# Kernel tuning notes

Measured on AMD Instinct MI355X. Metric: run time of the kernel, lower is better.

Reference implementation:

```python
import jax, jax.numpy as jnp
import numpy as np

HEADS = 16


def _linear(x, w, b):
    # torch nn.Linear: y = x @ W^T + b, W: (out, in)
    return jnp.einsum('bld,od->blo', x, w) + b


def setup_inputs() -> dict:
    key = jax.random.key(0)
    ks = jax.random.split(key, 11)
    B, L, QD, KVD = 8, 2048, 1024, 1024
    s_in = 1.0 / np.sqrt(QD)
    return {
        'query': jax.random.normal(ks[0], (B, L, QD), jnp.float32),
        'key':   jax.random.normal(ks[1], (B, L, KVD), jnp.float32),
        'value': jax.random.normal(ks[2], (B, L, KVD), jnp.float32),
        'wq_w': jax.random.normal(ks[3], (KVD, QD), jnp.float32) * s_in,
        'wq_b': jnp.zeros((KVD,), jnp.float32),
        'wk_w': jax.random.normal(ks[4], (KVD, KVD), jnp.float32) * s_in,
        'wk_b': jnp.zeros((KVD,), jnp.float32),
        'wv_w': jax.random.normal(ks[5], (KVD, KVD), jnp.float32) * s_in,
        'wv_b': jnp.zeros((KVD,), jnp.float32),
        'fo_w': jax.random.normal(ks[6], (QD, KVD), jnp.float32) * s_in,
        'fo_b': jnp.zeros((QD,), jnp.float32),
    }


def reference(query, key, value, wq_w, wq_b, wk_w, wk_b, wv_w, wv_b, fo_w, fo_b):
    B, Lq, _ = query.shape
    Lk = key.shape[1]
    kvd = wq_w.shape[0]
    head_dim = kvd // HEADS
    # reshape WITHOUT transpose, exactly as the torch source: (B, L, heads, head_dim)
    q = _linear(query, wq_w, wq_b).reshape(B, Lq, HEADS, head_dim)
    k = _linear(key,   wk_w, wk_b).reshape(B, Lk, HEADS, head_dim)
    v = _linear(value, wv_w, wv_b).reshape(B, Lk, HEADS, head_dim)
    scale = 1.0 / jnp.sqrt(jnp.float32(head_dim))
    # Faithful to source: seq axis acts as 'h'; heads axis is contracted (i,j).
    scores = jnp.einsum('bhid,bhjd->bhij', q, k) * scale  # (B, L, heads, heads)
    weights = jax.nn.softmax(scores, axis=-1)
    out = jnp.einsum('bhij,bhjd->bhid', weights, v)       # (B, L, heads, head_dim)
    out = out.reshape(B, Lq, kvd)
    return _linear(out, fo_w, fo_b)
```

## Files before the change

### kernel.cpp

```cpp
#include <hip/hip_runtime.h>
#include <hip/hip_bf16.h>


typedef __attribute__((ext_vector_type(8))) __bf16 bf16x8;
typedef __attribute__((ext_vector_type(4))) float f32x4;

#define BM 128
#define BN 128
#define BK 64

__device__ __forceinline__ float bf2f(ushort u) {
  union { unsigned int i; float f; } c; c.i = ((unsigned int)u) << 16; return c.f;
}
__device__ __forceinline__ ushort f2b(float f) {
  union { float f; unsigned int i; } c; c.f = f;
  unsigned int x = c.i;
  return (ushort)((x + 0x7FFFu + ((x >> 16) & 1u)) >> 16);
}

__global__ __launch_bounds__(256)
void cvt_f32_bf16(const float* __restrict__ s, ushort* __restrict__ d, int n8)
{
  int i = blockIdx.x * 256 + threadIdx.x;
  if (i >= n8) return;
  const float4* sp = reinterpret_cast<const float4*>(s) + (size_t)i * 2;
  float4 a = sp[0], b = sp[1];
  ushort u[8] = { f2b(a.x), f2b(a.y), f2b(a.z), f2b(a.w),
                  f2b(b.x), f2b(b.y), f2b(b.z), f2b(b.w) };
  reinterpret_cast<uint4*>(d)[i] = *reinterpret_cast<uint4*>(u);
}

__global__ __launch_bounds__(256)
void cvt_w3(const float* __restrict__ a, const float* __restrict__ b,
            const float* __restrict__ c, ushort* __restrict__ dst, int n8each)
{
  int i = blockIdx.x * 256 + threadIdx.x;
  if (i >= 3 * n8each) return;
  const float* s; int j;
  if (i < n8each)            { s = a; j = i; }
  else if (i < 2 * n8each)   { s = b; j = i - n8each; }
  else                       { s = c; j = i - 2 * n8each; }
  const float4* sp = reinterpret_cast<const float4*>(s) + (size_t)j * 2;
  float4 x = sp[0], y = sp[1];
  ushort u[8] = { f2b(x.x), f2b(x.y), f2b(x.z), f2b(x.w),
                  f2b(y.x), f2b(y.y), f2b(y.z), f2b(y.w) };
  reinterpret_cast<uint4*>(dst)[i] = *reinterpret_cast<uint4*>(u);
}

__global__ __launch_bounds__(256)
void cvt_wo_perm(const float* __restrict__ w, ushort* __restrict__ o)
{
  int t = blockIdx.x * 256 + threadIdx.x;
  int n  = t >> 7;
  int i8 = (t & 127) << 3;
  int blk = i8 >> 8, g = (i8 >> 6) & 3, c = (i8 >> 2) & 15;
  const float* src = w + (size_t)n * 1024 + 4 * g * 64 + blk * 16 + c;
  ushort u[8];
  #pragma unroll
  for (int j = 0; j < 8; ++j)
    u[j] = f2b(src[(j & 3) * 64 + (j >> 2)]);
  *reinterpret_cast<uint4*>(o + (size_t)n * 1024 + i8) = *reinterpret_cast<uint4*>(u);
}

template<int CMODE>
__global__ __launch_bounds__(512, 2)
void gemm8p(const ushort* __restrict__ A, const ushort* __restrict__ Bw,
            const float* __restrict__ bias, void* __restrict__ Cv,
            int M, int N, int K)
{
  extern __shared__ ushort lds[];

  const int tid  = threadIdx.x;
  const int lane = tid & 63;
  const int wid  = tid >> 6;
  const int wm   = wid >> 2;
  const int wn   = wid & 3;

  const int nwg = gridDim.x * gridDim.y;
  int fid = blockIdx.y * gridDim.x + blockIdx.x;
  if ((nwg & 7) == 0) fid = (fid & 7) * (nwg >> 3) + (fid >> 3);
  const int bx = fid % gridDim.x;
  const int by = fid / gridDim.x;
  const int m0 = by * 256, n0 = bx * 256;

  const int NT = K >> 6;

  const int csw = ((lane & 7) ^ (lane >> 3)) << 3;
  auto STAGE = [&](int h, int kt, int b) {
    const ushort* base = (h >= 2) ? Bw : A;
    const int o0 = (h >= 2) ? n0 : m0;
    const int rl = (h & 1) * 128;
    #pragma unroll
    for (int j = 0; j < 2; ++j) {
      int rt = rl + j * 64 + wid * 8;
      const ushort* src = base + (size_t)(o0 + rt + (lane >> 3)) * K + kt * 64 + csw;
      ushort* dst = lds + b * 32768 + (h >= 2 ? 16384 : 0) + rt * 64;
      __builtin_amdgcn_global_load_lds(
          (const __attribute__((address_space(1))) void*)src,
          (__attribute__((address_space(3))) void*)dst, 16, 0, 0);
    }
  };

  auto LDA = [&](int b, int mi, int kk) -> bf16x8 {
    int row  = (mi & 3) * 16 + wm * 64 + (mi >> 2) * 128 + (lane & 15);
    int slot = kk * 4 + (lane >> 4);
    int byte = row * 128 + (((slot ^ (row & 7)) & 7) << 4);
    return *reinterpret_cast<const bf16x8*>((const char*)(lds + b * 32768) + byte);
  };
  auto LDB = [&](int b, int ni, int kk) -> bf16x8 {
    int row  = (ni & 1) * 16 + wn * 32 + (ni >> 1) * 128 + (lane & 15);
    int slot = kk * 4 + (lane >> 4);
    int byte = row * 128 + (((slot ^ (row & 7)) & 7) << 4);
    return *reinterpret_cast<const bf16x8*>((const char*)(lds + b * 32768 + 16384) + byte);
  };

  f32x4 acc[8][4] = {};
  bf16x8 af[4][2], bf[4][2];

  STAGE(0, 0, 0); STAGE(2, 0, 0); STAGE(3, 0, 0); STAGE(1, 0, 0);
  asm volatile("s_waitcnt vmcnt(4)" ::: "memory");
  __builtin_amdgcn_s_barrier();

  for (int t = 0; t < NT; ++t) {
    const int cur = t & 1;
    const int nxt = cur ^ 1;
    const bool pf = (t + 1) < NT;

    #pragma unroll
    for (int i = 0; i < 4; ++i) { af[i][0] = LDA(cur, i, 0); af[i][1] = LDA(cur, i, 1); }
    #pragma unroll
    for (int n = 0; n < 2; ++n) { bf[n][0] = LDB(cur, n, 0); bf[n][1] = LDB(cur, n, 1); }
    if (pf) { STAGE(0, t + 1, nxt); asm volatile("s_waitcnt vmcnt(4)" ::: "memory"); }
    else    {                       asm volatile("s_waitcnt vmcnt(2)" ::: "memory"); }
    __builtin_amdgcn_s_barrier();
    asm volatile("s_waitcnt lgkmcnt(0)" ::: "memory");
    __builtin_amdgcn_sched_barrier(0);
    __builtin_amdgcn_s_setprio(1);
    #pragma unroll
    for (int i = 0; i < 4; ++i)
      #pragma unroll
      for (int n = 0; n < 2; ++n)
        #pragma unroll
        for (int kk = 0; kk < 2; ++kk)
          acc[i][n] = __builtin_amdgcn_mfma_f32_16x16x32_bf16(af[i][kk], bf[n][kk], acc[i][n], 0, 0, 0);
    __builtin_amdgcn_s_setprio(0);
    __builtin_amdgcn_s_barrier();

    #pragma unroll
    for (int n = 0; n < 2; ++n) { bf[2 + n][0] = LDB(cur, 2 + n, 0); bf[2 + n][1] = LDB(cur, 2 + n, 1); }
    if (pf) { STAGE(2, t + 1, nxt); asm volatile("s_waitcnt vmcnt(4)" ::: "memory"); }
    else    {                       asm volatile("s_waitcnt vmcnt(0)" ::: "memory"); }
    __builtin_amdgcn_s_barrier();
    asm volatile("s_waitcnt lgkmcnt(0)" ::: "memory");
    __builtin_amdgcn_sched_barrier(0);
    __builtin_amdgcn_s_setprio(1);
    #pragma unroll
    for (int i = 0; i < 4; ++i)
      #pragma unroll
      for (int n = 0; n < 2; ++n)
        #pragma unroll
        for (int kk = 0; kk < 2; ++kk)
          acc[i][2 + n] = __builtin_amdgcn_mfma_f32_16x16x32_bf16(af[i][kk], bf[2 + n][kk], acc[i][2 + n], 0, 0, 0);
    __builtin_amdgcn_s_setprio(0);
    __builtin_amdgcn_s_barrier();

    #pragma unroll
    for (int i = 0; i < 4; ++i) { af[i][0] = LDA(cur, 4 + i, 0); af[i][1] = LDA(cur, 4 + i, 1); }
    if (pf) STAGE(3, t + 1, nxt);
    __builtin_amdgcn_s_barrier();
    asm volatile("s_waitcnt lgkmcnt(0)" ::: "memory");
    __builtin_amdgcn_sched_barrier(0);
    __builtin_amdgcn_s_setprio(1);
    #pragma unroll
    for (int i = 0; i < 4; ++i)
      #pragma unroll
      for (int n = 0; n < 2; ++n)
        #pragma unroll
        for (int kk = 0; kk < 2; ++kk)
          acc[4 + i][n] = __builtin_amdgcn_mfma_f32_16x16x32_bf16(af[i][kk], bf[n][kk], acc[4 + i][n], 0, 0, 0);
    __builtin_amdgcn_s_setprio(0);
    __builtin_amdgcn_s_barrier();

    if (pf) { STAGE(1, t + 1, nxt); asm volatile("s_waitcnt vmcnt(4)" ::: "memory"); }
    __builtin_amdgcn_s_barrier();
    __builtin_amdgcn_s_setprio(1);
    #pragma unroll
    for (int i = 0; i < 4; ++i)
      #pragma unroll
      for (int n = 0; n < 2; ++n)
        #pragma unroll
        for (int kk = 0; kk < 2; ++kk)
          acc[4 + i][2 + n] = __builtin_amdgcn_mfma_f32_16x16x32_bf16(af[i][kk], bf[2 + n][kk], acc[4 + i][2 + n], 0, 0, 0);
    __builtin_amdgcn_s_setprio(0);
    __builtin_amdgcn_s_barrier();
  }

  #pragma unroll
  for (int ni = 0; ni < 4; ++ni) {
    int col = n0 + (ni & 1) * 16 + wn * 32 + (ni >> 1) * 128 + (lane & 15);
    float bv = bias[col];
    #pragma unroll
    for (int mi = 0; mi < 8; ++mi) {
      int row0 = m0 + (mi & 3) * 16 + wm * 64 + (mi >> 2) * 128 + ((lane >> 4) << 2);
      #pragma unroll
      for (int q = 0; q < 4; ++q) {
        float v = acc[mi][ni][q] + bv;
        if constexpr (CMODE == 0)
          ((float*)Cv)[(size_t)(row0 + q) * N + col] = v;
        else
          ((ushort*)Cv)[(size_t)(row0 + q) * N + col] = f2b(v);
      }
    }
  }
}

__global__ __launch_bounds__(256)
void attn_mfma2(const ushort* __restrict__ Q, const ushort* __restrict__ Kh,
                const ushort* __restrict__ V, ushort* __restrict__ Ot, int P)
{
  const int lane = threadIdx.x & 63;
  const int wid  = threadIdx.x >> 6;
  const int g = lane >> 4, c = lane & 15;
  const int stride = gridDim.x * 4;

  for (int p = blockIdx.x * 4 + wid; p < P; p += stride) {
    const ushort* qb = Q  + (size_t)p * 1024;
    const ushort* kb = Kh + (size_t)p * 1024;
    const ushort* vb = V  + (size_t)p * 1024;

    bf16x8 qf0 = *reinterpret_cast<const bf16x8*>(qb + c * 64 + g * 8);
    bf16x8 qf1 = *reinterpret_cast<const bf16x8*>(qb + c * 64 + 32 + g * 8);
    bf16x8 kf0 = *reinterpret_cast<const bf16x8*>(kb + c * 64 + g * 8);
    bf16x8 kf1 = *reinterpret_cast<const bf16x8*>(kb + c * 64 + 32 + g * 8);

    f32x4 s = {};
    s = __builtin_amdgcn_mfma_f32_16x16x32_bf16(kf0, qf0, s, 0, 0, 0);
    s = __builtin_amdgcn_mfma_f32_16x16x32_bf16(kf1, qf1, s, 0, 0, 0);

    float s0 = s[0] * 0.125f, s1 = s[1] * 0.125f;
    float s2 = s[2] * 0.125f, s3 = s[3] * 0.125f;
    float m = fmaxf(fmaxf(s0, s1), fmaxf(s2, s3));
    m = fmaxf(m, __shfl_xor(m, 16));
    m = fmaxf(m, __shfl_xor(m, 32));
    float e0 = __expf(s0 - m), e1 = __expf(s1 - m);
    float e2 = __expf(s2 - m), e3 = __expf(s3 - m);
    float sum = e0 + e1 + e2 + e3;
    sum += __shfl_xor(sum, 16);
    sum += __shfl_xor(sum, 32);
    float r = 1.0f / sum;

    uint pk0 = (uint)f2b(e0 * r) | ((uint)f2b(e1 * r) << 16);
    uint pk1 = (uint)f2b(e2 * r) | ((uint)f2b(e3 * r) << 16);

    int srcA = (((2 * g) & 3) << 4) | c;
    int srcB = (((2 * g + 1) & 3) << 4) | c;
    uint a0 = (uint)__shfl((int)pk0, srcA);
    uint a1 = (uint)__shfl((int)pk1, srcA);
    uint a2 = (uint)__shfl((int)pk0, srcB);
    uint a3 = (uint)__shfl((int)pk1, srcB);
    if (g >= 2) { a0 = 0; a1 = 0; a2 = 0; a3 = 0; }
    union { uint u[4]; bf16x8 v; } pa;
    pa.u[0] = a0; pa.u[1] = a1; pa.u[2] = a2; pa.u[3] = a3;

    ushort* ob = Ot + (size_t)p * 1024;
    #pragma unroll
    for (int blk = 0; blk < 4; ++blk) {
      union { ushort u[8]; bf16x8 v; } vf;
      #pragma unroll
      for (int e = 0; e < 8; ++e)
        vf.u[e] = vb[(8 * (g & 1) + e) * 64 + blk * 16 + c];
      f32x4 o = {};
      o = __builtin_amdgcn_mfma_f32_16x16x32_bf16(pa.v, vf.v, o, 0, 0, 0);
      uint lo = (uint)f2b(o[0]) | ((uint)f2b(o[1]) << 16);
      uint hi = (uint)f2b(o[2]) | ((uint)f2b(o[3]) << 16);
      uint2 w2; w2.x = lo; w2.y = hi;
      *reinterpret_cast<uint2*>(ob + blk * 256 + g * 64 + c * 4) = w2;
    }
  }
}

template<bool A_IS_BF16, bool OUT_BF16>
__global__ __launch_bounds__(256)
void gemm_bt(const void* __restrict__ Av, const float* __restrict__ B,
             const float* __restrict__ bias, void* __restrict__ Cv,
             int M, int N, int K)
{
  __shared__ ushort As[BM * BK];
  __shared__ ushort Bs[BN * BK];

  const int tid  = threadIdx.x;
  const int lane = tid & 63;
  const int wid  = tid >> 6;
  const int wr   = wid >> 1;
  const int wc   = wid & 1;
  const int m0   = blockIdx.y * BM;
  const int n0   = blockIdx.x * BN;

  f32x4 acc[4][4] = {};

  const int r   = tid >> 1;
  const int seg = (tid & 1) * 32;

  for (int k0 = 0; k0 < K; k0 += BK) {
    {
      ushort tmp[32];
      if constexpr (A_IS_BF16) {
        const ushort* gA = (const ushort*)Av + (size_t)(m0 + r) * K + k0 + seg;
        #pragma unroll
        for (int u = 0; u < 4; ++u)
          *reinterpret_cast<uint4*>(&tmp[u * 8]) =
              *reinterpret_cast<const uint4*>(gA + u * 8);
      } else {
        const float* gA = (const float*)Av + (size_t)(m0 + r) * K + k0 + seg;
        #pragma unroll
        for (int u = 0; u < 8; ++u) {
          float4 f = *reinterpret_cast<const float4*>(gA + u * 4);
          tmp[u * 4 + 0] = f2b(f.x); tmp[u * 4 + 1] = f2b(f.y);
          tmp[u * 4 + 2] = f2b(f.z); tmp[u * 4 + 3] = f2b(f.w);
        }
      }
      #pragma unroll
      for (int s4 = 0; s4 < 4; ++s4) {
        int slot = (seg >> 3) + s4;
        int byte = r * 128 + ((slot ^ (r & 7)) << 4);
        *reinterpret_cast<uint4*>((char*)As + byte) =
            *reinterpret_cast<uint4*>(&tmp[s4 * 8]);
      }
    }
    {
      const float* gB = B + (size_t)(n0 + r) * K + k0 + seg;
      ushort tmp[32];
      #pragma unroll
      for (int u = 0; u < 8; ++u) {
        float4 f = *reinterpret_cast<const float4*>(gB + u * 4);
        tmp[u * 4 + 0] = f2b(f.x); tmp[u * 4 + 1] = f2b(f.y);
        tmp[u * 4 + 2] = f2b(f.z); tmp[u * 4 + 3] = f2b(f.w);
      }
      #pragma unroll
      for (int s4 = 0; s4 < 4; ++s4) {
        int slot = (seg >> 3) + s4;
        int byte = r * 128 + ((slot ^ (r & 7)) << 4);
        *reinterpret_cast<uint4*>((char*)Bs + byte) =
            *reinterpret_cast<uint4*>(&tmp[s4 * 8]);
      }
    }
    __syncthreads();

    #pragma unroll
    for (int kk = 0; kk < 2; ++kk) {
      const int kbase = kk * 32 + ((lane >> 4) << 3);
      const int slot  = kbase >> 3;
      bf16x8 af[4], bfr[4];
      #pragma unroll
      for (int mi = 0; mi < 4; ++mi) {
        int row = wr * 64 + mi * 16 + (lane & 15);
        af[mi] = *reinterpret_cast<const bf16x8*>(
            (const char*)As + row * 128 + ((slot ^ (row & 7)) << 4));
      }
      #pragma unroll
      for (int ni = 0; ni < 4; ++ni) {
        int row = wc * 64 + ni * 16 + (lane & 15);
        bfr[ni] = *reinterpret_cast<const bf16x8*>(
            (const char*)Bs + row * 128 + ((slot ^ (row & 7)) << 4));
      }
      #pragma unroll
      for (int mi = 0; mi < 4; ++mi)
        #pragma unroll
        for (int ni = 0; ni < 4; ++ni)
          acc[mi][ni] = __builtin_amdgcn_mfma_f32_16x16x32_bf16(
              af[mi], bfr[ni], acc[mi][ni], 0, 0, 0);
    }
    __syncthreads();
  }

  #pragma unroll
  for (int ni = 0; ni < 4; ++ni) {
    int col = n0 + wc * 64 + ni * 16 + (lane & 15);
    float bv = bias[col];
    #pragma unroll
    for (int mi = 0; mi < 4; ++mi) {
      int row0 = m0 + wr * 64 + mi * 16 + ((lane >> 4) << 2);
      #pragma unroll
      for (int q = 0; q < 4; ++q) {
        float v = acc[mi][ni][q] + bv;
        if constexpr (OUT_BF16)
          ((ushort*)Cv)[(size_t)(row0 + q) * N + col] = f2b(v);
        else
          ((float*)Cv)[(size_t)(row0 + q) * N + col] = v;
      }
    }
  }
}

__global__ __launch_bounds__(256)
void attn_kernel(const ushort* __restrict__ Q, const ushort* __restrict__ Kh,
                 const ushort* __restrict__ V, ushort* __restrict__ O)
{
  __shared__ float smem[4][3][16][68];
  const int tid  = threadIdx.x;
  const int wid  = tid >> 6;
  const int lane = tid & 63;
  const size_t p = (size_t)blockIdx.x * 4 + wid;

  {
    const ushort* srcs[3] = { Q + p * 1024, Kh + p * 1024, V + p * 1024 };
    const int i  = lane >> 2;
    const int d0 = (lane & 3) * 16;
    #pragma unroll
    for (int m = 0; m < 3; ++m) {
      const ushort* s = srcs[m] + lane * 16;
      ushort u[16];
      *reinterpret_cast<uint4*>(&u[0]) = *reinterpret_cast<const uint4*>(s);
      *reinterpret_cast<uint4*>(&u[8]) = *reinterpret_cast<const uint4*>(s + 8);
      #pragma unroll
      for (int e = 0; e < 16; ++e) smem[wid][m][i][d0 + e] = bf2f(u[e]);
    }
  }
  __syncthreads();

  const int i  = lane >> 2;
  const int jg = lane & 3;
  const float* qrow = smem[wid][0][i];
  const float* k0r = smem[wid][1][jg * 4 + 0];
  const float* k1r = smem[wid][1][jg * 4 + 1];
  const float* k2r = smem[wid][1][jg * 4 + 2];
  const float* k3r = smem[wid][1][jg * 4 + 3];

  float s0 = 0.f, s1 = 0.f, s2 = 0.f, s3 = 0.f;
  #pragma unroll
  for (int d = 0; d < 64; ++d) {
    float qv = qrow[d];
    s0 += qv * k0r[d]; s1 += qv * k1r[d];
    s2 += qv * k2r[d]; s3 += qv * k3r[d];
  }
  const float scale = 0.125f;
  s0 *= scale; s1 *= scale; s2 *= scale; s3 *= scale;

  float mx = fmaxf(fmaxf(s0, s1), fmaxf(s2, s3));
  mx = fmaxf(mx, __shfl_xor(mx, 1));
  mx = fmaxf(mx, __shfl_xor(mx, 2));
  float e0 = __expf(s0 - mx), e1 = __expf(s1 - mx);
  float e2 = __expf(s2 - mx), e3 = __expf(s3 - mx);
  float sum = e0 + e1 + e2 + e3;
  sum += __shfl_xor(sum, 1);
  sum += __shfl_xor(sum, 2);
  float inv = 1.0f / sum;
  e0 *= inv; e1 *= inv; e2 *= inv; e3 *= inv;

  const float* v0r = smem[wid][2][jg * 4 + 0];
  const float* v1r = smem[wid][2][jg * 4 + 1];
  const float* v2r = smem[wid][2][jg * 4 + 2];
  const float* v3r = smem[wid][2][jg * 4 + 3];
  ushort* orow = O + p * 1024 + i * 64;

  #pragma unroll
  for (int cc = 0; cc < 4; ++cc) {
    float po[16];
    #pragma unroll
    for (int dd = 0; dd < 16; ++dd) {
      int d = cc * 16 + dd;
      po[dd] = e0 * v0r[d] + e1 * v1r[d] + e2 * v2r[d] + e3 * v3r[d];
    }
    #pragma unroll
    for (int dd = 0; dd < 16; ++dd) {
      po[dd] += __shfl_xor(po[dd], 1);
      po[dd] += __shfl_xor(po[dd], 2);
    }
    if (jg == cc) {
      #pragma unroll
      for (int dd = 0; dd < 16; ++dd) orow[cc * 16 + dd] = f2b(po[dd]);
    }
  }
}

extern "C" void kernel_launch(void* const* d_in, const int* in_sizes, int n_in,
                              void* d_out, int out_size, void* d_ws, size_t ws_size,
                              hipStream_t stream)
{
  const float* query = (const float*)d_in[0];
  const float* key_  = (const float*)d_in[1];
  const float* value = (const float*)d_in[2];
  const float* wq_w  = (const float*)d_in[3];
  const float* wq_b  = (const float*)d_in[4];
  const float* wk_w  = (const float*)d_in[5];
  const float* wk_b  = (const float*)d_in[6];
  const float* wv_w  = (const float*)d_in[7];
  const float* wv_b  = (const float*)d_in[8];
  const float* fo_w  = (const float*)d_in[9];
  const float* fo_b  = (const float*)d_in[10];

  const int K = 1024, N = 1024;
  const int M = in_sizes[0] / K;
  const size_t slot = (size_t)M * N;
  const size_t wsl  = (size_t)N * K;
  const size_t need = (4 * slot + 4 * wsl) * sizeof(ushort);

  if (ws_size >= need && (M % 256) == 0 && N == 1024 && K == 1024) {
    hipFuncSetAttribute(reinterpret_cast<const void*>(gemm8p<0>),
                        hipFuncAttributeMaxDynamicSharedMemorySize, 131072);
    hipFuncSetAttribute(reinterpret_cast<const void*>(gemm8p<1>),
                        hipFuncAttributeMaxDynamicSharedMemorySize, 131072);

    ushort* S0 = (ushort*)d_ws;
    ushort* S1 = S0 + slot;
    ushort* S2 = S1 + slot;
    ushort* S3 = S2 + slot;
    ushort* Wq = S3 + slot;
    ushort* Wo = Wq + 3 * wsl;

    const int n8w = (int)(wsl / 8);
    const int n8s = (int)(slot / 8);
    dim3 g8(N / 256, M / 256);
    dim3 b8(512);

    cvt_w3<<<dim3((3 * n8w + 255) / 256), dim3(256), 0, stream>>>(
        wq_w, wk_w, wv_w, Wq, n8w);
    cvt_wo_perm<<<dim3(512), dim3(256), 0, stream>>>(fo_w, Wo);

    cvt_f32_bf16<<<dim3((n8s + 255) / 256), dim3(256), 0, stream>>>(query, S0, n8s);
    gemm8p<1><<<g8, b8, 131072, stream>>>(S0, Wq,           wq_b, S1, M, N, K);
    cvt_f32_bf16<<<dim3((n8s + 255) / 256), dim3(256), 0, stream>>>(key_, S0, n8s);
    gemm8p<1><<<g8, b8, 131072, stream>>>(S0, Wq + wsl,     wk_b, S2, M, N, K);
    cvt_f32_bf16<<<dim3((n8s + 255) / 256), dim3(256), 0, stream>>>(value, S0, n8s);
    gemm8p<1><<<g8, b8, 131072, stream>>>(S0, Wq + 2 * wsl, wv_b, S3, M, N, K);

    attn_mfma2<<<dim3(2048), dim3(256), 0, stream>>>(S1, S2, S3, S0, M);
    gemm8p<0><<<g8, b8, 131072, stream>>>(S0, Wo, fo_b, d_out, M, N, K);
  } else {
    dim3 grid(N / BN, M / BM);
    ushort* Qb = (ushort*)d_ws;
    ushort* Kb = Qb + slot;
    ushort* Vb = Kb + slot;
    ushort* Ob = Vb + slot;
    gemm_bt<false, true><<<grid, dim3(256), 0, stream>>>(query, wq_w, wq_b, Qb, M, N, K);
    gemm_bt<false, true><<<grid, dim3(256), 0, stream>>>(key_,  wk_w, wk_b, Kb, M, N, K);
    gemm_bt<false, true><<<grid, dim3(256), 0, stream>>>(value, wv_w, wv_b, Vb, M, N, K);
    attn_kernel<<<dim3(M / 4), dim3(256), 0, stream>>>(Qb, Kb, Vb, Ob);
    gemm_bt<true, false><<<grid, dim3(256), 0, stream>>>(Ob, fo_w, fo_b, d_out, M, N, K);
  }
}
```

Before: 242.6 us.

## Batch Q/K/V input conversion and projection GEMMs into single launches

```diff
diff --git a/kernel.cpp b/kernel.cpp
--- a/kernel.cpp
+++ b/kernel.cpp
@@ -31,15 +31,32 @@
 }
 
 __global__ __launch_bounds__(256)
-void cvt_w3(const float* __restrict__ a, const float* __restrict__ b,
-            const float* __restrict__ c, ushort* __restrict__ dst, int n8each)
+void cvt_in3(const float* __restrict__ a, const float* __restrict__ b,
+             const float* __restrict__ c, ushort* __restrict__ dst, int n8each)
 {
   int i = blockIdx.x * 256 + threadIdx.x;
   if (i >= 3 * n8each) return;
   const float* s; int j;
-  if (i < n8each)            { s = a; j = i; }
-  else if (i < 2 * n8each)   { s = b; j = i - n8each; }
-  else                       { s = c; j = i - 2 * n8each; }
+  if (i < n8each)          { s = a; j = i; }
+  else if (i < 2 * n8each) { s = b; j = i - n8each; }
+  else                     { s = c; j = i - 2 * n8each; }
+  const float4* sp = reinterpret_cast<const float4*>(s) + (size_t)j * 2;
+  float4 x = sp[0], y = sp[1];
+  ushort u[8] = { f2b(x.x), f2b(x.y), f2b(x.z), f2b(x.w),
+                  f2b(y.x), f2b(y.y), f2b(y.z), f2b(y.w) };
+  reinterpret_cast<uint4*>(dst)[i] = *reinterpret_cast<uint4*>(u);
+}
+
+__global__ __launch_bounds__(256)
+void cvt_w3(const float* __restrict__ a, const float* __restrict__ b,
+            const float* __restrict__ c, ushort* __restrict__ dst, int n8each)
+{
+  int i = blockIdx.x * 256 + threadIdx.x;
+  if (i >= 3 * n8each) return;
+  const float* s; int j;
+  if (i < n8each)          { s = a; j = i; }
+  else if (i < 2 * n8each) { s = b; j = i - n8each; }
+  else                     { s = c; j = i - 2 * n8each; }
   const float4* sp = reinterpret_cast<const float4*>(s) + (size_t)j * 2;
   float4 x = sp[0], y = sp[1];
   ushort u[8] = { f2b(x.x), f2b(x.y), f2b(x.z), f2b(x.w),
@@ -63,13 +80,11 @@
 }
 
 template<int CMODE>
-__global__ __launch_bounds__(512, 2)
-void gemm8p(const ushort* __restrict__ A, const ushort* __restrict__ Bw,
-            const float* __restrict__ bias, void* __restrict__ Cv,
-            int M, int N, int K)
-{
-  extern __shared__ ushort lds[];
-
+__device__ __forceinline__
+void gemm_body(const ushort* __restrict__ A, const ushort* __restrict__ Bw,
+               const float* __restrict__ bias, void* __restrict__ Cv,
+               int N, int K, ushort* lds)
+{
   const int tid  = threadIdx.x;
   const int lane = tid & 63;
   const int wid  = tid >> 6;
@@ -212,6 +227,31 @@
       }
     }
   }
+}
+
+template<int CMODE>
+__global__ __launch_bounds__(512, 2)
+void gemm8p(const ushort* __restrict__ A, const ushort* __restrict__ Bw,
+            const float* __restrict__ bias, void* __restrict__ Cv,
+            int M, int N, int K)
+{
+  extern __shared__ ushort lds[];
+  gemm_body<CMODE>(A, Bw, bias, Cv, N, K, lds);
+}
+
+__global__ __launch_bounds__(512, 2)
+void gemm8p_qkv(const ushort* __restrict__ Abase, const ushort* __restrict__ Wbase,
+                const float* __restrict__ b0, const float* __restrict__ b1,
+                const float* __restrict__ b2, ushort* __restrict__ Cbase,
+                int M, int N, int K)
+{
+  extern __shared__ ushort lds[];
+  const int z = blockIdx.z;
+  const size_t slot = (size_t)M * K;
+  const size_t wsl  = (size_t)N * K;
+  const float* bias = (z == 0) ? b0 : (z == 1) ? b1 : b2;
+  gemm_body<1>(Abase + z * slot, Wbase + z * wsl, bias,
+               (void*)(Cbase + z * (size_t)M * N), N, K, lds);
 }
 
 __global__ __launch_bounds__(256)
@@ -493,9 +533,41 @@
   const int M = in_sizes[0] / K;
   const size_t slot = (size_t)M * N;
   const size_t wsl  = (size_t)N * K;
-  const size_t need = (4 * slot + 4 * wsl) * sizeof(ushort);
-
-  if (ws_size >= need && (M % 256) == 0 && N == 1024 && K == 1024) {
+  const size_t need_big = (6 * slot + 4 * wsl) * sizeof(ushort);
+  const size_t need_mid = (4 * slot + 4 * wsl) * sizeof(ushort);
+  const bool dims_ok = (M % 256) == 0 && N == 1024 && K == 1024;
+
+  const int n8w = (int)(wsl / 8);
+  const int n8s = (int)(slot / 8);
+
+  if (ws_size >= need_big && dims_ok) {
+    hipFuncSetAttribute(reinterpret_cast<const void*>(gemm8p<0>),
+                        hipFuncAttributeMaxDynamicSharedMemorySize, 131072);
+    hipFuncSetAttribute(reinterpret_cast<const void*>(gemm8p_qkv),
+                        hipFuncAttributeMaxDynamicSharedMemorySize, 131072);
+
+    ushort* I0 = (ushort*)d_ws;
+    ushort* P1 = I0 + 3 * slot;
+    ushort* Wq = P1 + 3 * slot;
+    ushort* Wo = Wq + 3 * wsl;
+    ushort* Ot = I0;
+
+    dim3 g8(N / 256, M / 256);
+    dim3 g8z(N / 256, M / 256, 3);
+    dim3 b8(512);
+
+    cvt_w3<<<dim3((3 * n8w + 255) / 256), dim3(256), 0, stream>>>(
+        wq_w, wk_w, wv_w, Wq, n8w);
+    cvt_wo_perm<<<dim3(512), dim3(256), 0, stream>>>(fo_w, Wo);
+    cvt_in3<<<dim3((3 * n8s + 255) / 256), dim3(256), 0, stream>>>(
+        query, key_, value, I0, n8s);
+
+    gemm8p_qkv<<<g8z, b8, 131072, stream>>>(I0, Wq, wq_b, wk_b, wv_b, P1, M, N, K);
+
+    attn_mfma2<<<dim3(2048), dim3(256), 0, stream>>>(
+        P1, P1 + slot, P1 + 2 * slot, Ot, M);
+    gemm8p<0><<<g8, b8, 131072, stream>>>(Ot, Wo, fo_b, d_out, M, N, K);
+  } else if (ws_size >= need_mid && dims_ok) {
     hipFuncSetAttribute(reinterpret_cast<const void*>(gemm8p<0>),
                         hipFuncAttributeMaxDynamicSharedMemorySize, 131072);
     hipFuncSetAttribute(reinterpret_cast<const void*>(gemm8p<1>),
@@ -508,8 +580,6 @@
     ushort* Wq = S3 + slot;
     ushort* Wo = Wq + 3 * wsl;
 
-    const int n8w = (int)(wsl / 8);
-    const int n8s = (int)(slot / 8);
     dim3 g8(N / 256, M / 256);
     dim3 b8(512);
 
```

Measured after the change: 242.5 us. Within noise of the previous version (-0.1%).

## Fuse fp32-to-bf16 input conversion into a batched QKV projection GEMM

Applied to the files above, without the earlier changes.

```diff
diff --git a/kernel.cpp b/kernel.cpp
--- a/kernel.cpp
+++ b/kernel.cpp
@@ -19,27 +19,15 @@
 }
 
 __global__ __launch_bounds__(256)
-void cvt_f32_bf16(const float* __restrict__ s, ushort* __restrict__ d, int n8)
-{
-  int i = blockIdx.x * 256 + threadIdx.x;
-  if (i >= n8) return;
-  const float4* sp = reinterpret_cast<const float4*>(s) + (size_t)i * 2;
-  float4 a = sp[0], b = sp[1];
-  ushort u[8] = { f2b(a.x), f2b(a.y), f2b(a.z), f2b(a.w),
-                  f2b(b.x), f2b(b.y), f2b(b.z), f2b(b.w) };
-  reinterpret_cast<uint4*>(d)[i] = *reinterpret_cast<uint4*>(u);
-}
-
-__global__ __launch_bounds__(256)
 void cvt_w3(const float* __restrict__ a, const float* __restrict__ b,
             const float* __restrict__ c, ushort* __restrict__ dst, int n8each)
 {
   int i = blockIdx.x * 256 + threadIdx.x;
   if (i >= 3 * n8each) return;
   const float* s; int j;
-  if (i < n8each)            { s = a; j = i; }
-  else if (i < 2 * n8each)   { s = b; j = i - n8each; }
-  else                       { s = c; j = i - 2 * n8each; }
+  if (i < n8each)          { s = a; j = i; }
+  else if (i < 2 * n8each) { s = b; j = i - n8each; }
+  else                     { s = c; j = i - 2 * n8each; }
   const float4* sp = reinterpret_cast<const float4*>(s) + (size_t)j * 2;
   float4 x = sp[0], y = sp[1];
   ushort u[8] = { f2b(x.x), f2b(x.y), f2b(x.z), f2b(x.w),
@@ -62,11 +50,188 @@
   *reinterpret_cast<uint4*>(o + (size_t)n * 1024 + i8) = *reinterpret_cast<uint4*>(u);
 }
 
-template<int CMODE>
 __global__ __launch_bounds__(512, 2)
-void gemm8p(const ushort* __restrict__ A, const ushort* __restrict__ Bw,
-            const float* __restrict__ bias, void* __restrict__ Cv,
-            int M, int N, int K)
+void gemm_qkvf(const float* __restrict__ Q, const float* __restrict__ Kin,
+               const float* __restrict__ Vin, const ushort* __restrict__ Wbase,
+               const float* __restrict__ b0, const float* __restrict__ b1,
+               const float* __restrict__ b2, ushort* __restrict__ Cbase,
+               int M, int N, int K)
+{
+  extern __shared__ char ldsb[];
+
+  const int z = blockIdx.z;
+  const float* Af = (z == 0) ? Q : (z == 1) ? Kin : Vin;
+  const ushort* Bw = Wbase + (size_t)z * N * K;
+  const float* bias = (z == 0) ? b0 : (z == 1) ? b1 : b2;
+  ushort* Cv = Cbase + (size_t)z * M * N;
+
+  const int tid  = threadIdx.x;
+  const int lane = tid & 63;
+  const int wid  = tid >> 6;
+  const int wm   = wid >> 2;
+  const int wn   = wid & 3;
+
+  const int nwg = gridDim.x * gridDim.y;
+  int fid = blockIdx.y * gridDim.x + blockIdx.x;
+  if ((nwg & 7) == 0) fid = (fid & 7) * (nwg >> 3) + (fid >> 3);
+  const int bx = fid % gridDim.x;
+  const int by = fid / gridDim.x;
+  const int m0 = by * 256, n0 = bx * 256;
+
+  const int NT = K >> 6;
+
+  const int csw = ((lane & 7) ^ (lane >> 3)) << 3;
+  auto STAGE_B = [&](int h, int kt, int b) {
+    #pragma unroll
+    for (int j = 0; j < 2; ++j) {
+      int rt = h * 128 + j * 64 + wid * 8;
+      const ushort* src = Bw + (size_t)(n0 + rt + (lane >> 3)) * K + kt * 64 + csw;
+      char* dst = ldsb + 65536 + b * 32768 + rt * 128;
+      __builtin_amdgcn_global_load_lds(
+          (const __attribute__((address_space(1))) void*)src,
+          (__attribute__((address_space(3))) void*)dst, 16, 0, 0);
+    }
+  };
+  auto STAGE_A = [&](int h, int kt) {
+    const int rl = h * 128 + wid * 4 + (lane >> 4);
+    const int sl = lane & 15;
+    #pragma unroll
+    for (int u = 0; u < 4; ++u) {
+      int row = rl + u * 32;
+      const float* src = Af + (size_t)(m0 + row) * K + kt * 64
+                         + ((sl ^ (row & 15)) << 2);
+      char* dst = ldsb + h * 32768 + u * 8192 + wid * 1024;
+      __builtin_amdgcn_global_load_lds(
+          (const __attribute__((address_space(1))) void*)src,
+          (__attribute__((address_space(3))) void*)dst, 16, 0, 0);
+    }
+  };
+
+  auto LDAF = [&](int mi, int kk) -> bf16x8 {
+    int row = (mi & 3) * 16 + wm * 64 + (mi >> 2) * 128 + (lane & 15);
+    int s0  = kk * 8 + ((lane >> 4) << 1);
+    const float4 lo = *reinterpret_cast<const float4*>(
+        ldsb + row * 256 + (((s0)     ^ (row & 15)) << 4));
+    const float4 hi = *reinterpret_cast<const float4*>(
+        ldsb + row * 256 + (((s0 + 1) ^ (row & 15)) << 4));
+    uint u0, u1, u2, u3;
+    asm("v_cvt_pk_bf16_f32 %0, %1, %2" : "=v"(u0) : "v"(lo.x), "v"(lo.y));
+    asm("v_cvt_pk_bf16_f32 %0, %1, %2" : "=v"(u1) : "v"(lo.z), "v"(lo.w));
+    asm("v_cvt_pk_bf16_f32 %0, %1, %2" : "=v"(u2) : "v"(hi.x), "v"(hi.y));
+    asm("v_cvt_pk_bf16_f32 %0, %1, %2" : "=v"(u3) : "v"(hi.z), "v"(hi.w));
+    union { uint u[4]; bf16x8 v; } r;
+    r.u[0] = u0; r.u[1] = u1; r.u[2] = u2; r.u[3] = u3;
+    return r.v;
+  };
+  auto LDB = [&](int b, int ni, int kk) -> bf16x8 {
+    int row  = (ni & 1) * 16 + wn * 32 + (ni >> 1) * 128 + (lane & 15);
+    int slot = kk * 4 + (lane >> 4);
+    int byte = row * 128 + (((slot ^ (row & 7)) & 7) << 4);
+    return *reinterpret_cast<const bf16x8*>(ldsb + 65536 + b * 32768 + byte);
+  };
+
+  f32x4 acc[8][4] = {};
+  bf16x8 af[4][2], bf[4][2];
+
+  STAGE_B(0, 0, 0); STAGE_A(0, 0); STAGE_B(1, 0, 0); STAGE_A(1, 0);
+  asm volatile("s_waitcnt vmcnt(6)" ::: "memory");
+  __builtin_amdgcn_s_barrier();
+
+  for (int t = 0; t < NT; ++t) {
+    const int cur = t & 1;
+    const int nxt = cur ^ 1;
+    const bool pf = (t + 1) < NT;
+
+    if (pf) STAGE_B(0, t + 1, nxt);
+    #pragma unroll
+    for (int i = 0; i < 4; ++i) { af[i][0] = LDAF(i, 0); af[i][1] = LDAF(i, 1); }
+    #pragma unroll
+    for (int n = 0; n < 2; ++n) { bf[n][0] = LDB(cur, n, 0); bf[n][1] = LDB(cur, n, 1); }
+    if (pf) asm volatile("s_waitcnt vmcnt(6)" ::: "memory");
+    else    asm volatile("s_waitcnt vmcnt(4)" ::: "memory");
+    __builtin_amdgcn_s_barrier();
+    asm volatile("s_waitcnt lgkmcnt(0)" ::: "memory");
+    __builtin_amdgcn_sched_barrier(0);
+    __builtin_amdgcn_s_setprio(1);
+    #pragma unroll
+    for (int i = 0; i < 4; ++i)
+      #pragma unroll
+      for (int n = 0; n < 2; ++n)
+        #pragma unroll
+        for (int kk = 0; kk < 2; ++kk)
+          acc[i][n] = __builtin_amdgcn_mfma_f32_16x16x32_bf16(af[i][kk], bf[n][kk], acc[i][n], 0, 0, 0);
+    __builtin_amdgcn_s_setprio(0);
+    __builtin_amdgcn_s_barrier();
+
+    if (pf) STAGE_A(0, t + 1);
+    #pragma unroll
+    for (int n = 0; n < 2; ++n) { bf[2 + n][0] = LDB(cur, 2 + n, 0); bf[2 + n][1] = LDB(cur, 2 + n, 1); }
+    if (pf) asm volatile("s_waitcnt vmcnt(6)" ::: "memory");
+    else    asm volatile("s_waitcnt vmcnt(0)" ::: "memory");
+    __builtin_amdgcn_s_barrier();
+    asm volatile("s_waitcnt lgkmcnt(0)" ::: "memory");
+    __builtin_amdgcn_sched_barrier(0);
+    __builtin_amdgcn_s_setprio(1);
+    #pragma unroll
+    for (int i = 0; i < 4; ++i)
+      #pragma unroll
+      for (int n = 0; n < 2; ++n)
+        #pragma unroll
+        for (int kk = 0; kk < 2; ++kk)
+          acc[i][2 + n] = __builtin_amdgcn_mfma_f32_16x16x32_bf16(af[i][kk], bf[2 + n][kk], acc[i][2 + n], 0, 0, 0);
+    __builtin_amdgcn_s_setprio(0);
+    __builtin_amdgcn_s_barrier();
+
+    if (pf) STAGE_B(1, t + 1, nxt);
+    #pragma unroll
+    for (int i = 0; i < 4; ++i) { af[i][0] = LDAF(4 + i, 0); af[i][1] = LDAF(4 + i, 1); }
+    __builtin_amdgcn_s_barrier();
+    asm volatile("s_waitcnt lgkmcnt(0)" ::: "memory");
+    __builtin_amdgcn_sched_barrier(0);
+    __builtin_amdgcn_s_setprio(1);
+    #pragma unroll
+    for (int i = 0; i < 4; ++i)
+      #pragma unroll
+      for (int n = 0; n < 2; ++n)
+        #pragma unroll
+        for (int kk = 0; kk < 2; ++kk)
+          acc[4 + i][n] = __builtin_amdgcn_mfma_f32_16x16x32_bf16(af[i][kk], bf[n][kk], acc[4 + i][n], 0, 0, 0);
+    __builtin_amdgcn_s_setprio(0);
+    __builtin_amdgcn_s_barrier();
+
+    if (pf) { STAGE_A(1, t + 1);
+              asm volatile("s_waitcnt vmcnt(6)" ::: "memory"); }
+    __builtin_amdgcn_s_barrier();
+    __builtin_amdgcn_s_setprio(1);
+    #pragma unroll
+    for (int i = 0; i < 4; ++i)
+      #pragma unroll
+      for (int n = 0; n < 2; ++n)
+        #pragma unroll
+        for (int kk = 0; kk < 2; ++kk)
+          acc[4 + i][2 + n] = __builtin_amdgcn_mfma_f32_16x16x32_bf16(af[i][kk], bf[2 + n][kk], acc[4 + i][2 + n], 0, 0, 0);
+    __builtin_amdgcn_s_setprio(0);
+    __builtin_amdgcn_s_barrier();
+  }
+
+  #pragma unroll
+  for (int ni = 0; ni < 4; ++ni) {
+    int col = n0 + (ni & 1) * 16 + wn * 32 + (ni >> 1) * 128 + (lane & 15);
+    float bv = bias[col];
+    #pragma unroll
+    for (int mi = 0; mi < 8; ++mi) {
+      int row0 = m0 + (mi & 3) * 16 + wm * 64 + (mi >> 2) * 128 + ((lane >> 4) << 2);
+      #pragma unroll
+      for (int q = 0; q < 4; ++q)
+        Cv[(size_t)(row0 + q) * N + col] = f2b(acc[mi][ni][q] + bv);
+    }
+  }
+}
+
+__global__ __launch_bounds__(512, 2)
+void gemm8p_f32out(const ushort* __restrict__ A, const ushort* __restrict__ Bw,
+                   const float* __restrict__ bias, float* __restrict__ Cv,
+                   int M, int N, int K)
 {
   extern __shared__ ushort lds[];
 
@@ -203,13 +368,8 @@
     for (int mi = 0; mi < 8; ++mi) {
       int row0 = m0 + (mi & 3) * 16 + wm * 64 + (mi >> 2) * 128 + ((lane >> 4) << 2);
       #pragma unroll
-      for (int q = 0; q < 4; ++q) {
-        float v = acc[mi][ni][q] + bv;
-        if constexpr (CMODE == 0)
-          ((float*)Cv)[(size_t)(row0 + q) * N + col] = v;
-        else
-          ((ushort*)Cv)[(size_t)(row0 + q) * N + col] = f2b(v);
-      }
+      for (int q = 0; q < 4; ++q)
+        Cv[(size_t)(row0 + q) * N + col] = acc[mi][ni][q] + bv;
     }
   }
 }
@@ -494,38 +654,35 @@
   const size_t slot = (size_t)M * N;
   const size_t wsl  = (size_t)N * K;
   const size_t need = (4 * slot + 4 * wsl) * sizeof(ushort);
-
-  if (ws_size >= need && (M % 256) == 0 && N == 1024 && K == 1024) {
-    hipFuncSetAttribute(reinterpret_cast<const void*>(gemm8p<0>),
+  const bool dims_ok = (M % 256) == 0 && N == 1024 && K == 1024;
+
+  const int n8w = (int)(wsl / 8);
+
+  if (ws_size >= need && dims_ok) {
+    hipFuncSetAttribute(reinterpret_cast<const void*>(gemm_qkvf),
                         hipFuncAttributeMaxDynamicSharedMemorySize, 131072);
-    hipFuncSetAttribute(reinterpret_cast<const void*>(gemm8p<1>),
+    hipFuncSetAttribute(reinterpret_cast<const void*>(gemm8p_f32out),
                         hipFuncAttributeMaxDynamicSharedMemorySize, 131072);
 
-    ushort* S0 = (ushort*)d_ws;
-    ushort* S1 = S0 + slot;
-    ushort* S2 = S1 + slot;
-    ushort* S3 = S2 + slot;
-    ushort* Wq = S3 + slot;
+    ushort* Ot = (ushort*)d_ws;
+    ushort* P1 = Ot + slot;
+    ushort* Wq = P1 + 3 * slot;
     ushort* Wo = Wq + 3 * wsl;
 
-    const int n8w = (int)(wsl / 8);
-    const int n8s = (int)(slot / 8);
     dim3 g8(N / 256, M / 256);
+    dim3 g8z(N / 256, M / 256, 3);
     dim3 b8(512);
 
     cvt_w3<<<dim3((3 * n8w + 255) / 256), dim3(256), 0, stream>>>(
         wq_w, wk_w, wv_w, Wq, n8w);
     cvt_wo_perm<<<dim3(512), dim3(256), 0, stream>>>(fo_w, Wo);
 
-    cvt_f32_bf16<<<dim3((n8s + 255) / 256), dim3(256), 0, stream>>>(query, S0, n8s);
-    gemm8p<1><<<g8, b8, 131072, stream>>>(S0, Wq,           wq_b, S1, M, N, K);
-    cvt_f32_bf16<<<dim3((n8s + 255) / 256), dim3(256), 0, stream>>>(key_, S0, n8s);
-    gemm8p<1><<<g8, b8, 131072, stream>>>(S0, Wq + wsl,     wk_b, S2, M, N, K);
-    cvt_f32_bf16<<<dim3((n8s + 255) / 256), dim3(256), 0, stream>>>(value, S0, n8s);
-    gemm8p<1><<<g8, b8, 131072, stream>>>(S0, Wq + 2 * wsl, wv_b, S3, M, N, K);
-
-    attn_mfma2<<<dim3(2048), dim3(256), 0, stream>>>(S1, S2, S3, S0, M);
-    gemm8p<0><<<g8, b8, 131072, stream>>>(S0, Wo, fo_b, d_out, M, N, K);
+    gemm_qkvf<<<g8z, b8, 131072, stream>>>(query, key_, value, Wq,
+                                           wq_b, wk_b, wv_b, P1, M, N, K);
+
+    attn_mfma2<<<dim3(2048), dim3(256), 0, stream>>>(
+        P1, P1 + slot, P1 + 2 * slot, Ot, M);
+    gemm8p_f32out<<<g8, b8, 131072, stream>>>(Ot, Wo, fo_b, (float*)d_out, M, N, K);
   } else {
     dim3 grid(N / BN, M / BM);
     ushort* Qb = (ushort*)d_ws;
```

Measured after the change: 253.6 us. 1.05x slower.
